# Performance work log

Hardware: AMD Instinct MI355X
Metric: run time of the kernel (lower is better)

Reference implementation:

```python
import jax, jax.numpy as jnp
import numpy as np

B, N, C_FEAT = 2, 1024, 64
S, K, K_FP = 512, 32, 3
D_MODEL, N_HEAD = 128, 4
EPS_BN = 1e-5


def square_distance(src, dst):
    # src [B,N,3], dst [B,M,3] -> [B,N,M], same expansion as torch version
    d = -2.0 * jnp.einsum('bnc,bmc->bnm', src, dst)
    d = d + jnp.sum(src ** 2, -1)[:, :, None]
    d = d + jnp.sum(dst ** 2, -1)[:, None, :]
    return d


def gather_points(points, idx):
    # points [B,N,C], idx [B,...] int -> [B,...,C]  (index_points)
    return jax.vmap(lambda p, i: p[i])(points, idx)


def fps(xyz, n_samples):
    # furthest point sampling, deterministic start at index 0
    Bs, Np, _ = xyz.shape
    def step(carry, _):
        dist, far = carry
        centroid = jax.vmap(lambda p, i: p[i])(xyz, far)  # [B,3]
        d = jnp.sum((xyz - centroid[:, None, :]) ** 2, -1)
        dist = jnp.minimum(dist, d)
        new_far = jnp.argmax(dist, -1).astype(jnp.int32)
        return (dist, new_far), far
    init = (jnp.full((Bs, Np), 1e10, xyz.dtype), jnp.zeros((Bs,), jnp.int32))
    _, idxs = jax.lax.scan(step, init, None, length=n_samples)
    return idxs.T  # [B,S]


def knn(nsample, xyz, new_xyz):
    d = square_distance(new_xyz, xyz)
    _, idx = jax.lax.top_k(-d, nsample)
    return idx  # [B, n_query, nsample]


def setup_inputs() -> dict:
    key = jax.random.key(0)
    ks = jax.random.split(key, 12)
    Din = 2 * C_FEAT + 3  # 131 = 3 + 2*channels (PreExtraction in_channels)
    def lin(k, fan_in, shape):
        return (jax.random.normal(k, shape, jnp.float32) / np.sqrt(fan_in)).astype(jnp.float32)
    z = lambda n: jnp.zeros((n,), jnp.float32)
    return {
        'xyz': jax.random.normal(ks[0], (B, N, 3), jnp.float32),
        'feats': jax.random.normal(ks[1], (B, N, C_FEAT), jnp.float32),
        'affine_alpha': jnp.ones((1, 1, 1, C_FEAT + 3), jnp.float32),
        'affine_beta': jnp.zeros((1, 1, 1, C_FEAT + 3), jnp.float32),
        'W_t': lin(ks[2], Din, (Din, D_MODEL)), 'b_t': z(D_MODEL),
        'bn_g': jnp.ones((D_MODEL,), jnp.float32), 'bn_b': z(D_MODEL),
        'Wq': lin(ks[3], D_MODEL, (D_MODEL, D_MODEL)), 'bq': z(D_MODEL),
        'Wk': lin(ks[4], D_MODEL, (D_MODEL, D_MODEL)), 'bk': z(D_MODEL),
        'Wv': lin(ks[5], D_MODEL, (D_MODEL, D_MODEL)), 'bv': z(D_MODEL),
        'Wo': lin(ks[6], D_MODEL, (D_MODEL, D_MODEL)), 'bo': z(D_MODEL),
        'Wp1': lin(ks[7], 3, (3, D_MODEL)), 'bp1': z(D_MODEL),
        'Wp2': lin(ks[8], D_MODEL, (D_MODEL, N_HEAD)), 'bp2': z(N_HEAD),
    }


def reference(xyz, feats, affine_alpha, affine_beta, W_t, b_t, bn_g, bn_b,
              Wq, bq, Wk, bk, Wv, bv, Wo, bo, Wp1, bp1, Wp2, bp2):
    # ---- LocalGrouper (FPS + KNN + gather + center-normalize + affine) ----
    fps_idx = fps(xyz, S)                       # [B,S]
    new_xyz = gather_points(xyz, fps_idx)       # [B,S,3]
    anchor_feats = gather_points(feats, fps_idx)  # [B,S,C]
    idx = knn(K, xyz, new_xyz)                  # [B,S,K]
    grouped_xyz = gather_points(xyz, idx)       # [B,S,K,3]
    grouped_pts = gather_points(feats, idx)     # [B,S,K,C]
    grouped = jnp.concatenate([grouped_pts, grouped_xyz], -1)  # [B,S,K,C+3]
    mean = jnp.mean(grouped, axis=2, keepdims=True)
    std = jnp.std((grouped - mean).reshape(B, -1), axis=-1, ddof=1)[:, None, None, None]
    grouped = (grouped - mean) / (std + 1e-5)
    grouped = affine_alpha * grouped + affine_beta
    anchor_rep = jnp.broadcast_to(anchor_feats[:, :, None, :], (B, S, K, C_FEAT))
    new_points = jnp.concatenate([grouped, anchor_rep], -1)  # [B,S,K,2C+3]
    # ---- PreExtraction transfer (1x1 conv + BN(eval) + ReLU) + max over K ----
    y = jnp.einsum('bskd,do->bsko', new_points, W_t) + b_t
    y = y * (bn_g / jnp.sqrt(1.0 + EPS_BN)) + bn_b  # BN with running stats (0,1)
    y = jax.nn.relu(y)
    v_k = jnp.max(y, axis=2)                    # [B,S,D_MODEL]
    # ---- PointNetFeaturePropagation (KNN-3 inverse-distance interp) ----
    idx_fp = knn(K_FP, new_xyz, xyz)            # [B,N,3]
    sqrd = square_distance(xyz, new_xyz)        # [B,N,S]
    d_near = jnp.clip(jnp.take_along_axis(sqrd, idx_fp, axis=2), 1e-10, None)
    w = 1.0 / d_near
    w = w / jnp.sum(w, -1, keepdims=True)
    grouped_v = gather_points(v_k, idx_fp)      # [B,N,3,D]
    v_q = jnp.einsum('bnk,bnkc->bnc', w, grouped_v)  # [B,N,D]
    # ---- PointTransformerCrossAttention ----
    Dh = D_MODEL // N_HEAD
    qh = (v_q @ Wq + bq).reshape(B, N, N_HEAD, Dh)
    kh = (v_k @ Wk + bk).reshape(B, S, N_HEAD, Dh)
    vh = (v_k @ Wv + bv).reshape(B, S, N_HEAD, Dh)
    rel = xyz[:, :, None, :] - new_xyz[:, None, :, :]         # [B,N,S,3]
    rpe = jax.nn.relu(rel @ Wp1 + bp1) @ Wp2 + bp2            # [B,N,S,H]
    energy = jnp.einsum('bihd,bjhd->bhij', qh, kh) / jnp.sqrt(jnp.float32(Dh))
    attn = jax.nn.softmax(energy + rpe.transpose(0, 3, 1, 2), axis=-1)
    out = jnp.einsum('bhij,bjhd->bihd', attn, vh).reshape(B, N, D_MODEL)
    return out @ Wo + bo
```

## Files before the change

### kernel.cpp

```cpp
#include <hip/hip_runtime.h>
#include <math.h>

namespace {

constexpr int B  = 2;
constexpr int N  = 1024;
constexpr int CF = 64;
constexpr int S  = 512;
constexpr int K  = 32;
constexpr int DM = 128;
constexpr int NH = 4;
constexpr int DH = 32;
constexpr int GC = 67;
constexpr int DIN = 131;
constexpr int DPAD = 132;
constexpr int EPAD = 516;

typedef float f2 __attribute__((ext_vector_type(2)));

template <int CTRL>
__device__ inline float dpp_mov_f(float v) {
  return __int_as_float(__builtin_amdgcn_update_dpp(0, __float_as_int(v), CTRL, 0xF, 0xF, true));
}
template <int CTRL>
__device__ inline unsigned dpp_mov_self_u(unsigned v) {
  return (unsigned)__builtin_amdgcn_update_dpp((int)v, (int)v, CTRL, 0xF, 0xF, false);
}

__global__ void __launch_bounds__(64, 1)
fps_kernel(const float* __restrict__ xyz, int* __restrict__ fps_idx,
           float* __restrict__ new_xyz) {
  const int b = blockIdx.x;
  const int lane = threadIdx.x;
  __shared__ __align__(16) float4 pts4[N];
  __shared__ int farhist[S];
  for (int p = lane; p < N; p += 64) {
    pts4[p] = make_float4(xyz[b*N*3 + p*3+0], xyz[b*N*3 + p*3+1], xyz[b*N*3 + p*3+2], 0.0f);
  }
  __syncthreads();
  f2 X[8], Y[8], Z[8];
  float dist[16];
  #pragma unroll
  for (int j = 0; j < 8; ++j) {
    const float4 a = pts4[(2*j)*64 + lane];
    const float4 c = pts4[(2*j+1)*64 + lane];
    X[j] = f2{a.x, c.x}; Y[j] = f2{a.y, c.y}; Z[j] = f2{a.z, c.z};
  }
  #pragma unroll
  for (int k = 0; k < 16; ++k) dist[k] = 1e10f;
  int far = 0;
  for (int s = 0; s < S; ++s) {
    if (lane == 0) farhist[s] = far;
    const float4 c = pts4[far];
    const f2 cx = f2{c.x, c.x}, cy = f2{c.y, c.y}, cz = f2{c.z, c.z};
    #pragma unroll
    for (int j = 0; j < 8; ++j) {
      const f2 dx = X[j] - cx, dy = Y[j] - cy, dz = Z[j] - cz;
      const f2 q = dx*dx + dy*dy + dz*dz;
      dist[2*j]   = fminf(dist[2*j],   q.x);
      dist[2*j+1] = fminf(dist[2*j+1], q.y);
    }
    float m[8];
    #pragma unroll
    for (int j = 0; j < 8; ++j) m[j] = fmaxf(dist[j], dist[j+8]);
    #pragma unroll
    for (int j = 0; j < 4; ++j) m[j] = fmaxf(m[j], m[j+4]);
    float mv = fmaxf(fmaxf(m[0], m[2]), fmaxf(m[1], m[3]));
    mv = fmaxf(mv, dpp_mov_f<0x111>(mv));
    mv = fmaxf(mv, dpp_mov_f<0x112>(mv));
    mv = fmaxf(mv, dpp_mov_f<0x114>(mv));
    mv = fmaxf(mv, dpp_mov_f<0x118>(mv));
    mv = fmaxf(mv, dpp_mov_f<0x142>(mv));
    mv = fmaxf(mv, dpp_mov_f<0x143>(mv));
    const float maxv = __int_as_float(__builtin_amdgcn_readlane(__float_as_int(mv), 63));
    unsigned cnd[16];
    #pragma unroll
    for (int k = 0; k < 16; ++k) {
      cnd[k] = (dist[k] == maxv) ? (unsigned)(k*64 + lane) : 0xFFFFFFFFu;
    }
    #pragma unroll
    for (int k = 0; k < 8; ++k) cnd[k] = min(cnd[k], cnd[k+8]);
    #pragma unroll
    for (int k = 0; k < 4; ++k) cnd[k] = min(cnd[k], cnd[k+4]);
    unsigned cand = min(min(cnd[0], cnd[2]), min(cnd[1], cnd[3]));
    cand = min(cand, dpp_mov_self_u<0x111>(cand));
    cand = min(cand, dpp_mov_self_u<0x112>(cand));
    cand = min(cand, dpp_mov_self_u<0x114>(cand));
    cand = min(cand, dpp_mov_self_u<0x118>(cand));
    cand = min(cand, dpp_mov_self_u<0x142>(cand));
    cand = min(cand, dpp_mov_self_u<0x143>(cand));
    far = __builtin_amdgcn_readlane((int)cand, 63);
  }
  __syncthreads();
  for (int s = lane; s < S; s += 64) {
    const int f = farhist[s];
    const float4 c = pts4[f];
    fps_idx[b*S+s] = f;
    new_xyz[(b*S+s)*3+0] = c.x;
    new_xyz[(b*S+s)*3+1] = c.y;
    new_xyz[(b*S+s)*3+2] = c.z;
  }
}

__global__ void knn_kernel(const float* __restrict__ xyz, const float* __restrict__ new_xyz,
                           int* __restrict__ knn_idx) {
  const int b = blockIdx.y;
  const int tid = threadIdx.x;
  const int wave = tid >> 6, lane = tid & 63;
  const int s = blockIdx.x * 4 + wave;
  __shared__ float pts[N*3];
  for (int i = tid; i < N*3; i += 256) pts[i] = xyz[b*N*3 + i];
  __syncthreads();
  const float qx = new_xyz[(b*S+s)*3+0], qy = new_xyz[(b*S+s)*3+1], qz = new_xyz[(b*S+s)*3+2];
  const float qn = qx*qx + qy*qy + qz*qz;
  float d[16];
  #pragma unroll
  for (int j = 0; j < 16; ++j) {
    const int p = j*64 + lane;
    const float px = pts[p*3+0], py = pts[p*3+1], pz = pts[p*3+2];
    const float dot = qx*px + qy*py + qz*pz;
    const float pn  = px*px + py*py + pz*pz;
    d[j] = (-2.0f*dot + qn) + pn;
  }
  unsigned mask = 0xFFFFu;
  for (int k = 0; k < K; ++k) {
    float bv = INFINITY; int bj = 0;
    #pragma unroll
    for (int j = 0; j < 16; ++j) {
      if (((mask >> j) & 1u) && d[j] < bv) { bv = d[j]; bj = j; }
    }
    int bp = bj*64 + lane;
    #pragma unroll
    for (int m = 1; m < 64; m <<= 1) {
      const float ov = __shfl_xor(bv, m);
      const int   op = __shfl_xor(bp, m);
      if (ov < bv || (ov == bv && op < bp)) { bv = ov; bp = op; }
    }
    if (lane == 0) knn_idx[(b*S+s)*K + k] = bp;
    if ((bp & 63) == lane) mask &= ~(1u << (bp >> 6));
  }
}

__global__ void group_stats_kernel(const float* __restrict__ feats, const float* __restrict__ xyz,
                                   const int* __restrict__ knn_idx, float* __restrict__ mean_out,
                                   float2* __restrict__ partials) {
  const int bs = blockIdx.x;
  const int b = bs / S;
  const int t = threadIdx.x;
  __shared__ int sidx[K];
  if (t < K) sidx[t] = knn_idx[bs*K + t];
  __syncthreads();
  float v[K];
  float ls = 0.0f, lsq = 0.0f;
  if (t < GC) {
    float sum = 0.0f;
    #pragma unroll
    for (int k = 0; k < K; ++k) {
      const int p = sidx[k];
      const float g = (t < CF) ? feats[(b*N+p)*CF + t] : xyz[(b*N+p)*3 + (t-CF)];
      v[k] = g; sum += g;
    }
    const float mean = sum * (1.0f/K);
    mean_out[bs*GC + t] = mean;
    #pragma unroll
    for (int k = 0; k < K; ++k) {
      const float c = v[k] - mean;
      ls += c; lsq += c*c;
    }
  }
  __shared__ float r1[128], r2[128];
  r1[t] = ls; r2[t] = lsq;
  __syncthreads();
  for (int off = 64; off >= 1; off >>= 1) {
    if (t < off) { r1[t] += r1[t+off]; r2[t] += r2[t+off]; }
    __syncthreads();
  }
  if (t == 0) partials[bs] = make_float2(r1[0], r2[0]);
}

__global__ void stats_kernel(const float2* __restrict__ partials, float* __restrict__ invstd) {
  const int b = blockIdx.x;
  const int lane = threadIdx.x;
  double su = 0.0, sq = 0.0;
  for (int i = lane; i < S; i += 64) {
    const float2 p = partials[b*S+i];
    su += (double)p.x; sq += (double)p.y;
  }
  #pragma unroll
  for (int m = 1; m < 64; m <<= 1) { su += __shfl_xor(su, m); sq += __shfl_xor(sq, m); }
  if (lane == 0) {
    const double nn = (double)S * K * GC;
    const double var = (sq - su*su/nn) / (nn - 1.0);
    invstd[b] = 1.0f / ((float)sqrt(var) + 1e-5f);
  }
}

__global__ void transfer_kernel(const float* __restrict__ feats, const float* __restrict__ xyz,
                                const int* __restrict__ knn_idx, const int* __restrict__ fps_idx,
                                const float* __restrict__ mean_in, const float* __restrict__ invstd,
                                const float* __restrict__ alpha, const float* __restrict__ beta,
                                const float* __restrict__ W_t, const float* __restrict__ b_t,
                                const float* __restrict__ bn_g, const float* __restrict__ bn_b,
                                float* __restrict__ v_k) {
  const int bs = blockIdx.x;
  const int b = bs / S;
  const int t = threadIdx.x;
  __shared__ __align__(16) float np_s[K][DPAD];
  __shared__ int sidx[K];
  __shared__ int sanchor;
  if (t < K) sidx[t] = knn_idx[bs*K + t];
  if (t == 0) sanchor = fps_idx[bs];
  __syncthreads();
  const float sinv = invstd[b];
  for (int k = 0; k < K; ++k) {
    const int p = sidx[k];
    for (int c = t; c < DPAD; c += 128) {
      float val = 0.0f;
      if (c < GC) {
        const float g = (c < CF) ? feats[(b*N+p)*CF + c] : xyz[(b*N+p)*3 + (c-CF)];
        val = (g - mean_in[bs*GC + c]) * sinv * alpha[c] + beta[c];
      } else if (c < DIN) {
        val = feats[(b*N+sanchor)*CF + (c - GC)];
      }
      np_s[k][c] = val;
    }
  }
  __syncthreads();
  float acc[K];
  const float bt = b_t[t];
  #pragma unroll
  for (int k = 0; k < K; ++k) acc[k] = bt;
  for (int d4 = 0; d4 < DPAD/4; ++d4) {
    const int d = d4*4;
    const float w0 = W_t[(d+0)*DM + t];
    const float w1 = W_t[(d+1)*DM + t];
    const float w2 = W_t[(d+2)*DM + t];
    const float w3 = (d+3 < DIN) ? W_t[(d+3)*DM + t] : 0.0f;
    #pragma unroll
    for (int k = 0; k < K; ++k) {
      const float4 f = *reinterpret_cast<const float4*>(&np_s[k][d]);
      acc[k] = acc[k] + f.x*w0 + f.y*w1 + f.z*w2 + f.w*w3;
    }
  }
  const float scale = bn_g[t] / sqrtf(1.0f + 1e-5f);
  const float shift = bn_b[t];
  float mx = -INFINITY;
  #pragma unroll
  for (int k = 0; k < K; ++k) {
    const float y = fmaxf(acc[k]*scale + shift, 0.0f);
    mx = fmaxf(mx, y);
  }
  v_k[bs*DM + t] = mx;
}

__global__ void interp_kernel(const float* __restrict__ xyz, const float* __restrict__ new_xyz,
                              const float* __restrict__ v_k, float* __restrict__ v_q) {
  const int b = blockIdx.y;
  const int tid = threadIdx.x;
  const int wave = tid >> 6, lane = tid & 63;
  const int n = blockIdx.x*4 + wave;
  __shared__ float pts[S*3];
  for (int i = tid; i < S*3; i += 256) pts[i] = new_xyz[b*S*3 + i];
  __syncthreads();
  const float qx = xyz[(b*N+n)*3+0], qy = xyz[(b*N+n)*3+1], qz = xyz[(b*N+n)*3+2];
  const float qn = qx*qx + qy*qy + qz*qz;
  float d[8];
  #pragma unroll
  for (int j = 0; j < 8; ++j) {
    const int p = j*64 + lane;
    const float px = pts[p*3+0], py = pts[p*3+1], pz = pts[p*3+2];
    const float dot = qx*px + qy*py + qz*pz;
    const float pn  = px*px + py*py + pz*pz;
    d[j] = (-2.0f*dot + qn) + pn;
  }
  unsigned mask = 0xFFu;
  float sd[3]; int sp[3];
  #pragma unroll
  for (int k = 0; k < 3; ++k) {
    float bv = INFINITY; int bj = 0;
    #pragma unroll
    for (int j = 0; j < 8; ++j) {
      if (((mask >> j) & 1u) && d[j] < bv) { bv = d[j]; bj = j; }
    }
    int bp = bj*64 + lane;
    #pragma unroll
    for (int m = 1; m < 64; m <<= 1) {
      const float ov = __shfl_xor(bv, m);
      const int   op = __shfl_xor(bp, m);
      if (ov < bv || (ov == bv && op < bp)) { bv = ov; bp = op; }
    }
    sd[k] = bv; sp[k] = bp;
    if ((bp & 63) == lane) mask &= ~(1u << (bp >> 6));
  }
  float w0 = 1.0f / fmaxf(sd[0], 1e-10f);
  float w1 = 1.0f / fmaxf(sd[1], 1e-10f);
  float w2 = 1.0f / fmaxf(sd[2], 1e-10f);
  const float wsum = w0 + w1 + w2;
  w0 /= wsum; w1 /= wsum; w2 /= wsum;
  const float* vk0 = v_k + (b*S + sp[0])*DM;
  const float* vk1 = v_k + (b*S + sp[1])*DM;
  const float* vk2 = v_k + (b*S + sp[2])*DM;
  #pragma unroll
  for (int c = lane; c < DM; c += 64) {
    v_q[(b*N+n)*DM + c] = w0*vk0[c] + w1*vk1[c] + w2*vk2[c];
  }
}

__global__ void linear_fused_kernel(const float* __restrict__ vq, const float* __restrict__ vk,
                                    const float* __restrict__ Wq, const float* __restrict__ bq,
                                    const float* __restrict__ Wk, const float* __restrict__ bk,
                                    const float* __restrict__ Wv, const float* __restrict__ bv,
                                    float* __restrict__ qbuf, float* __restrict__ kpb,
                                    float* __restrict__ vpb) {
  const int r = blockIdx.x;
  const int t = threadIdx.x;
  __shared__ float rin[DM];
  if (r < B*N) {
    rin[t] = vq[r*DM + t];
    __syncthreads();
    float acc = bq[t];
    for (int d = 0; d < DM; ++d) acc += rin[d] * Wq[d*DM + t];
    qbuf[r*DM + t] = acc;
  } else {
    const int rk = r - B*N;
    rin[t] = vk[rk*DM + t];
    __syncthreads();
    float acck = bk[t], accv = bv[t];
    for (int d = 0; d < DM; ++d) {
      const float f = rin[d];
      acck += f * Wk[d*DM + t];
      accv += f * Wv[d*DM + t];
    }
    kpb[rk*DM + t] = acck;
    vpb[rk*DM + t] = accv;
  }
}

__global__ void attn_kernel(const float* __restrict__ xyz, const float* __restrict__ new_xyz,
                            const float* __restrict__ qb, const float* __restrict__ kp,
                            const float* __restrict__ vp, const float* __restrict__ Wp1,
                            const float* __restrict__ bp1, const float* __restrict__ Wp2,
                            const float* __restrict__ bp2, const float* __restrict__ Wo,
                            const float* __restrict__ bo, float* __restrict__ out) {
  const int bn = blockIdx.x;
  const int b = bn / N;
  const int t = threadIdx.x;
  __shared__ __align__(16) float e[NH][EPAD];
  __shared__ float qn_s[DM];
  __shared__ float oa[DM];
  __shared__ float ssum[NH];
  qn_s[t] = qb[bn*DM + t];
  __syncthreads();
  const float qx = xyz[bn*3+0], qy = xyz[bn*3+1], qz = xyz[bn*3+2];
  const float rs = 0.17677669529663687f;
  for (int j = t; j < S; j += 128) {
    const float px = new_xyz[(b*S+j)*3+0], py = new_xyz[(b*S+j)*3+1], pz = new_xyz[(b*S+j)*3+2];
    const float rx = qx-px, ry = qy-py, rz = qz-pz;
    float r0 = bp2[0], r1 = bp2[1], r2 = bp2[2], r3 = bp2[3];
    for (int m = 0; m < DM; ++m) {
      float hm = rx*Wp1[m] + ry*Wp1[DM+m] + rz*Wp1[2*DM+m] + bp1[m];
      hm = fmaxf(hm, 0.0f);
      r0 += hm*Wp2[m*NH+0]; r1 += hm*Wp2[m*NH+1];
      r2 += hm*Wp2[m*NH+2]; r3 += hm*Wp2[m*NH+3];
    }
    const float rpe[NH] = {r0, r1, r2, r3};
    #pragma unroll
    for (int h = 0; h < NH; ++h) {
      const float* kr = kp + (b*S+j)*DM + h*DH;
      const float* qr = qn_s + h*DH;
      float acc = 0.0f;
      #pragma unroll
      for (int dd = 0; dd < DH; ++dd) acc += qr[dd]*kr[dd];
      e[h][j] = acc*rs + rpe[h];
    }
  }
  __syncthreads();
  const int h = t >> 5, g = t & 31;
  float mx = -INFINITY;
  for (int j = g; j < S; j += 32) mx = fmaxf(mx, e[h][j]);
  #pragma unroll
  for (int m = 16; m >= 1; m >>= 1) mx = fmaxf(mx, __shfl_xor(mx, m));
  float sum = 0.0f;
  for (int j = g; j < S; j += 32) { const float ex = expf(e[h][j]-mx); e[h][j] = ex; sum += ex; }
  #pragma unroll
  for (int m = 16; m >= 1; m >>= 1) sum += __shfl_xor(sum, m);
  if (g == 0) ssum[h] = sum;
  __syncthreads();
  float acc = 0.0f;
  for (int j = 0; j < S; j += 4) {
    const float4 ev = *reinterpret_cast<const float4*>(&e[h][j]);
    acc += ev.x * vp[(b*S+j+0)*DM + t];
    acc += ev.y * vp[(b*S+j+1)*DM + t];
    acc += ev.z * vp[(b*S+j+2)*DM + t];
    acc += ev.w * vp[(b*S+j+3)*DM + t];
  }
  oa[t] = acc / ssum[h];
  __syncthreads();
  float facc = bo[t];
  for (int d = 0; d < DM; ++d) facc += oa[d] * Wo[d*DM + t];
  out[bn*DM + t] = facc;
}

}

extern "C" void kernel_launch(void* const* d_in, const int* in_sizes, int n_in,
                              void* d_out, int out_size, void* d_ws, size_t ws_size,
                              hipStream_t stream) {
  const float* xyz   = (const float*)d_in[0];
  const float* feats = (const float*)d_in[1];
  const float* alpha = (const float*)d_in[2];
  const float* beta  = (const float*)d_in[3];
  const float* W_t   = (const float*)d_in[4];
  const float* b_t   = (const float*)d_in[5];
  const float* bn_g  = (const float*)d_in[6];
  const float* bn_b  = (const float*)d_in[7];
  const float* Wq = (const float*)d_in[8];  const float* bq = (const float*)d_in[9];
  const float* Wk = (const float*)d_in[10]; const float* bk = (const float*)d_in[11];
  const float* Wv = (const float*)d_in[12]; const float* bv = (const float*)d_in[13];
  const float* Wo = (const float*)d_in[14]; const float* bo = (const float*)d_in[15];
  const float* Wp1= (const float*)d_in[16]; const float* bp1= (const float*)d_in[17];
  const float* Wp2= (const float*)d_in[18]; const float* bp2= (const float*)d_in[19];

  char* w = (char*)d_ws;
  int*    fps_i = (int*)   (w + 0);
  float*  nxyz  = (float*) (w + 4096);
  int*    knn_i = (int*)   (w + 16384);
  float*  meanb = (float*) (w + 147456);
  float2* part  = (float2*)(w + 421888);
  float*  invs  = (float*) (w + 430080);
  float*  vk    = (float*) (w + 430336);
  float*  vq    = (float*) (w + 954624);
  float*  qbuf  = (float*) (w + 2003200);
  float*  kpb   = (float*) (w + 3051776);
  float*  vpb   = (float*) (w + 3576064);
  float*  outf  = (float*)d_out;

  fps_kernel<<<B, 64, 0, stream>>>(xyz, fps_i, nxyz);
  knn_kernel<<<dim3(S/4, B), 256, 0, stream>>>(xyz, nxyz, knn_i);
  group_stats_kernel<<<B*S, 128, 0, stream>>>(feats, xyz, knn_i, meanb, part);
  stats_kernel<<<B, 64, 0, stream>>>(part, invs);
  transfer_kernel<<<B*S, 128, 0, stream>>>(feats, xyz, knn_i, fps_i, meanb, invs,
                                           alpha, beta, W_t, b_t, bn_g, bn_b, vk);
  interp_kernel<<<dim3(N/4, B), 256, 0, stream>>>(xyz, nxyz, vk, vq);
  linear_fused_kernel<<<B*N + B*S, 128, 0, stream>>>(vq, vk, Wq, bq, Wk, bk, Wv, bv,
                                                     qbuf, kpb, vpb);
  attn_kernel<<<B*N, 128, 0, stream>>>(xyz, nxyz, qbuf, kpb, vpb, Wp1, bp1, Wp2, bp2, Wo, bo, outf);
}
```

Baseline: 453.9 us.

## Fuse K/V and Q projections into transfer and interp kernels, use 3-input reductions

Measured after the change: 452.7 us. No clear change (-0.2%).

```diff
diff --git a/kernel.cpp b/kernel.cpp
--- a/kernel.cpp
+++ b/kernel.cpp
@@ -18,6 +18,9 @@
 
 typedef float f2 __attribute__((ext_vector_type(2)));
 
+__device__ inline float max3f(float a, float b, float c) { return fmaxf(fmaxf(a, b), c); }
+__device__ inline unsigned min3u(unsigned a, unsigned b, unsigned c) { return min(min(a, b), c); }
+
 template <int CTRL>
 __device__ inline float dpp_mov_f(float v) {
   return __int_as_float(__builtin_amdgcn_update_dpp(0, __float_as_int(v), CTRL, 0xF, 0xF, true));
@@ -60,12 +63,12 @@
       dist[2*j]   = fminf(dist[2*j],   q.x);
       dist[2*j+1] = fminf(dist[2*j+1], q.y);
     }
-    float m[8];
-    #pragma unroll
-    for (int j = 0; j < 8; ++j) m[j] = fmaxf(dist[j], dist[j+8]);
-    #pragma unroll
-    for (int j = 0; j < 4; ++j) m[j] = fmaxf(m[j], m[j+4]);
-    float mv = fmaxf(fmaxf(m[0], m[2]), fmaxf(m[1], m[3]));
+    const float l0 = max3f(dist[0],  dist[1],  dist[2]);
+    const float l1 = max3f(dist[3],  dist[4],  dist[5]);
+    const float l2 = max3f(dist[6],  dist[7],  dist[8]);
+    const float l3 = max3f(dist[9],  dist[10], dist[11]);
+    const float l4 = max3f(dist[12], dist[13], dist[14]);
+    float mv = fmaxf(max3f(l0, l1, l2), max3f(l3, l4, dist[15]));
     mv = fmaxf(mv, dpp_mov_f<0x111>(mv));
     mv = fmaxf(mv, dpp_mov_f<0x112>(mv));
     mv = fmaxf(mv, dpp_mov_f<0x114>(mv));
@@ -78,11 +81,12 @@
     for (int k = 0; k < 16; ++k) {
       cnd[k] = (dist[k] == maxv) ? (unsigned)(k*64 + lane) : 0xFFFFFFFFu;
     }
-    #pragma unroll
-    for (int k = 0; k < 8; ++k) cnd[k] = min(cnd[k], cnd[k+8]);
-    #pragma unroll
-    for (int k = 0; k < 4; ++k) cnd[k] = min(cnd[k], cnd[k+4]);
-    unsigned cand = min(min(cnd[0], cnd[2]), min(cnd[1], cnd[3]));
+    const unsigned u0 = min3u(cnd[0],  cnd[1],  cnd[2]);
+    const unsigned u1 = min3u(cnd[3],  cnd[4],  cnd[5]);
+    const unsigned u2 = min3u(cnd[6],  cnd[7],  cnd[8]);
+    const unsigned u3 = min3u(cnd[9],  cnd[10], cnd[11]);
+    const unsigned u4 = min3u(cnd[12], cnd[13], cnd[14]);
+    unsigned cand = min(min3u(u0, u1, u2), min3u(u3, u4, cnd[15]));
     cand = min(cand, dpp_mov_self_u<0x111>(cand));
     cand = min(cand, dpp_mov_self_u<0x112>(cand));
     cand = min(cand, dpp_mov_self_u<0x114>(cand));
@@ -201,11 +205,15 @@
                                 const float* __restrict__ alpha, const float* __restrict__ beta,
                                 const float* __restrict__ W_t, const float* __restrict__ b_t,
                                 const float* __restrict__ bn_g, const float* __restrict__ bn_b,
-                                float* __restrict__ v_k) {
+                                const float* __restrict__ Wk, const float* __restrict__ bk,
+                                const float* __restrict__ Wv, const float* __restrict__ bv,
+                                float* __restrict__ v_k, float* __restrict__ kpb,
+                                float* __restrict__ vpb) {
   const int bs = blockIdx.x;
   const int b = bs / S;
   const int t = threadIdx.x;
   __shared__ __align__(16) float np_s[K][DPAD];
+  __shared__ float vrow[DM];
   __shared__ int sidx[K];
   __shared__ int sanchor;
   if (t < K) sidx[t] = knn_idx[bs*K + t];
@@ -251,16 +259,28 @@
     mx = fmaxf(mx, y);
   }
   v_k[bs*DM + t] = mx;
+  vrow[t] = mx;
+  __syncthreads();
+  float acck = bk[t], accv = bv[t];
+  for (int d = 0; d < DM; ++d) {
+    const float f = vrow[d];
+    acck += f * Wk[d*DM + t];
+    accv += f * Wv[d*DM + t];
+  }
+  kpb[bs*DM + t] = acck;
+  vpb[bs*DM + t] = accv;
 }
 
 __global__ void interp_kernel(const float* __restrict__ xyz, const float* __restrict__ new_xyz,
-                              const float* __restrict__ v_k, float* __restrict__ v_q) {
+                              const float* __restrict__ v_k, const float* __restrict__ Wq,
+                              const float* __restrict__ bq, float* __restrict__ qbuf) {
   const int b = blockIdx.y;
   const int tid = threadIdx.x;
   const int wave = tid >> 6, lane = tid & 63;
   const int n = blockIdx.x*4 + wave;
   __shared__ float pts[S*3];
-  for (int i = tid; i < S*3; i += 256) pts[i] = new_xyz[b*S*3 + i];
+  __shared__ float vqs[4][DM];
+  for (int i = tid; i < S*3; i += 256) pts[i] = xyz ? new_xyz[b*S*3 + i] : 0.0f;
   __syncthreads();
   const float qx = xyz[(b*N+n)*3+0], qy = xyz[(b*N+n)*3+1], qz = xyz[(b*N+n)*3+2];
   const float qn = qx*qx + qy*qy + qz*qz;
@@ -302,37 +322,16 @@
   const float* vk2 = v_k + (b*S + sp[2])*DM;
   #pragma unroll
   for (int c = lane; c < DM; c += 64) {
-    v_q[(b*N+n)*DM + c] = w0*vk0[c] + w1*vk1[c] + w2*vk2[c];
-  }
-}
-
-__global__ void linear_fused_kernel(const float* __restrict__ vq, const float* __restrict__ vk,
-                                    const float* __restrict__ Wq, const float* __restrict__ bq,
-                                    const float* __restrict__ Wk, const float* __restrict__ bk,
-                                    const float* __restrict__ Wv, const float* __restrict__ bv,
-                                    float* __restrict__ qbuf, float* __restrict__ kpb,
-                                    float* __restrict__ vpb) {
-  const int r = blockIdx.x;
-  const int t = threadIdx.x;
-  __shared__ float rin[DM];
-  if (r < B*N) {
-    rin[t] = vq[r*DM + t];
-    __syncthreads();
-    float acc = bq[t];
-    for (int d = 0; d < DM; ++d) acc += rin[d] * Wq[d*DM + t];
-    qbuf[r*DM + t] = acc;
-  } else {
-    const int rk = r - B*N;
-    rin[t] = vk[rk*DM + t];
-    __syncthreads();
-    float acck = bk[t], accv = bv[t];
-    for (int d = 0; d < DM; ++d) {
-      const float f = rin[d];
-      acck += f * Wk[d*DM + t];
-      accv += f * Wv[d*DM + t];
-    }
-    kpb[rk*DM + t] = acck;
-    vpb[rk*DM + t] = accv;
+    vqs[wave][c] = w0*vk0[c] + w1*vk1[c] + w2*vk2[c];
+  }
+  __syncthreads();
+  const float* row = vqs[wave];
+  #pragma unroll
+  for (int half = 0; half < 2; ++half) {
+    const int c = lane + half*64;
+    float acc = bq[c];
+    for (int d = 0; d < DM; ++d) acc += row[d] * Wq[d*DM + c];
+    qbuf[(b*N+n)*DM + c] = acc;
   }
 }
 
@@ -429,7 +428,6 @@
   float2* part  = (float2*)(w + 421888);
   float*  invs  = (float*) (w + 430080);
   float*  vk    = (float*) (w + 430336);
-  float*  vq    = (float*) (w + 954624);
   float*  qbuf  = (float*) (w + 2003200);
   float*  kpb   = (float*) (w + 3051776);
   float*  vpb   = (float*) (w + 3576064);
@@ -440,9 +438,8 @@
   group_stats_kernel<<<B*S, 128, 0, stream>>>(feats, xyz, knn_i, meanb, part);
   stats_kernel<<<B, 64, 0, stream>>>(part, invs);
   transfer_kernel<<<B*S, 128, 0, stream>>>(feats, xyz, knn_i, fps_i, meanb, invs,
-                                           alpha, beta, W_t, b_t, bn_g, bn_b, vk);
-  interp_kernel<<<dim3(N/4, B), 256, 0, stream>>>(xyz, nxyz, vk, vq);
-  linear_fused_kernel<<<B*N + B*S, 128, 0, stream>>>(vq, vk, Wq, bq, Wk, bk, Wv, bv,
-                                                     qbuf, kpb, vpb);
+                                           alpha, beta, W_t, b_t, bn_g, bn_b,
+                                           Wk, bk, Wv, bv, vk, kpb, vpb);
+  interp_kernel<<<dim3(N/4, B), 256, 0, stream>>>(xyz, nxyz, vk, Wq, bq, qbuf);
   attn_kernel<<<B*N, 128, 0, stream>>>(xyz, nxyz, qbuf, kpb, vpb, Wp1, bp1, Wp2, bp2, Wo, bo, outf);
 }
```
